# Kernel optimization log

Measured on AMD Instinct MI355X. Metric: run time of the kernel, lower is better.

The kernel has to match this reference:

```python
import jax, jax.numpy as jnp
import numpy as np

B_, L_ = 1, 1024
D_MODEL, D_INNER, D_XB = 2048, 4096, 1024
D_STATE = 16
DT_RANK = 128
INTER = 8192
EPS = 1e-5
GC = D_INNER // D_STATE   # 256 state groups (each covers D_STATE channels)
REP = D_INNER // D_XB     # 4: repeat_kv expansion factor for x and B


def setup_inputs() -> dict:
    key = jax.random.key(0)
    ks = jax.random.split(key, 8)
    s = 0.02
    return {
        "hidden_states": jax.random.normal(ks[0], (B_, L_, D_MODEL), jnp.float32),
        "rms1_w": jnp.ones((D_MODEL,), jnp.float32),
        "in_proj_w": jax.random.normal(ks[1], (2 * D_INNER + 2 * D_XB + DT_RANK, D_MODEL), jnp.float32) * s,
        "dt_proj_w": jax.random.normal(ks[2], (D_INNER, DT_RANK), jnp.float32) * s,
        "dt_proj_b": jax.random.normal(ks[3], (D_INNER,), jnp.float32) * 0.5 - 4.0,
        "A_log": jnp.tile(jnp.log(jnp.arange(1, D_STATE + 1, dtype=jnp.float32)), (D_INNER, 1)),
        "D_skip": jnp.ones((D_INNER,), jnp.float32),
        "out_proj_w": jax.random.normal(ks[4], (D_MODEL, D_INNER), jnp.float32) * s,
        "rms2_w": jnp.ones((D_MODEL,), jnp.float32),
        "gate_w": jax.random.normal(ks[5], (INTER, D_MODEL), jnp.float32) * s,
        "up_w": jax.random.normal(ks[6], (INTER, D_MODEL), jnp.float32) * s,
        "down_w": jax.random.normal(ks[7], (D_MODEL, INTER), jnp.float32) * s,
    }


def _rmsnorm(x, w):
    return x * jax.lax.rsqrt(jnp.mean(x * x, axis=-1, keepdims=True) + EPS) * w


def _mamba(x, in_proj_w, dt_proj_w, dt_proj_b, A_log, D_skip, out_proj_w):
    b, l, _ = x.shape
    zxbcdt = x @ in_proj_w.T  # (b,l, 2*d_inner + 2*d_xb + dt_rank)
    z = zxbcdt[..., :D_INNER]
    xv = zxbcdt[..., D_INNER:D_INNER + D_XB]
    Bm = zxbcdt[..., D_INNER + D_XB:D_INNER + 2 * D_XB]
    Cm = zxbcdt[..., D_INNER + 2 * D_XB:2 * D_INNER + 2 * D_XB]
    dt_in = zxbcdt[..., 2 * D_INNER + 2 * D_XB:]
    dt = jax.nn.softplus(dt_in @ dt_proj_w.T + dt_proj_b)  # (b,l,d_inner)
    # repeat_kv-style expansion of x and B from d_xb to d_inner (grouped by d_state)
    xg = jnp.repeat(xv.reshape(b, l, D_XB // D_STATE, D_STATE), REP, axis=2)  # (b,l,GC,n)
    Bg = jnp.repeat(Bm.reshape(b, l, D_XB // D_STATE, D_STATE), REP, axis=2)  # (b,l,GC,n)
    Cg = Cm.reshape(b, l, GC, D_STATE)                                        # (b,l,GC,n)
    x_full = xg.reshape(b, l, D_INNER)
    A = -jnp.exp(A_log)                       # (d_inner, n)
    dA = jnp.exp(dt[..., None] * A)           # (b,l,d_inner,n)
    dtx = (dt * x_full).reshape(b, l, GC, D_INNER // GC)  # channels per group == D_STATE here
    dBx = (dtx[..., :, None] * Bg[..., None, :]).reshape(b, l, D_INNER, D_STATE)

    def step(h, inp):
        dA_i, dBx_i, C_i = inp
        h = dA_i * h + dBx_i                  # (b,d_inner,n)
        # channel d in group d // D_STATE shares C of that group
        y = jnp.einsum('bgn,bgcn->bgc', C_i, h.reshape(b, GC, D_INNER // GC, D_STATE))
        return h, y.reshape(b, D_INNER)

    h0 = jnp.zeros((b, D_INNER, D_STATE), x.dtype)
    _, ys = jax.lax.scan(step, h0, (dA.transpose(1, 0, 2, 3), dBx.transpose(1, 0, 2, 3), Cg.transpose(1, 0, 2, 3)))
    y = ys.transpose(1, 0, 2) + D_skip * x_full
    y = y * jax.nn.silu(z)
    return y @ out_proj_w.T


def reference(hidden_states, rms1_w, in_proj_w, dt_proj_w, dt_proj_b, A_log, D_skip, out_proj_w, rms2_w, gate_w, up_w, down_w):
    res = hidden_states
    h = _rmsnorm(hidden_states, rms1_w)
    h = res + _mamba(h, in_proj_w, dt_proj_w, dt_proj_b, A_log, D_skip, out_proj_w)
    res = h
    hn = _rmsnorm(h, rms2_w)
    mlp = (jax.nn.silu(hn @ gate_w.T) * (hn @ up_w.T)) @ down_w.T
    return res + mlp
```

## Files before the change

kernel.cpp:

```cpp
#include <hip/hip_runtime.h>
#include <cstdint>
#include <cstddef>

#define L_SEQ   1024
#define DMODEL  2048
#define DINNER  4096
#define DXB     1024
#define DSTATE  16
#define DTRANK  128
#define INTER   8192
#define ZROW    10368
#define NCHUNK  16
#define CLEN    64

typedef __attribute__((ext_vector_type(8))) short  short8;
typedef __attribute__((ext_vector_type(4))) float  floatx4;
typedef unsigned short ushort_t;

__device__ __forceinline__ unsigned short f2bf(float f) {
  unsigned u = __float_as_uint(f);
  u += 0x7FFFu + ((u >> 16) & 1u);
  return (unsigned short)(u >> 16);
}
__device__ __forceinline__ float bf2f(unsigned short h) {
  return __uint_as_float(((unsigned)h) << 16);
}

__device__ __forceinline__ void gl_lds16(const void* g, void* l) {
  __builtin_amdgcn_global_load_lds(
      (const __attribute__((address_space(1))) unsigned int*)g,
      (__attribute__((address_space(3))) unsigned int*)l,
      16, 0, 0);
}

__global__ void __launch_bounds__(256) cvt_kernel(
    const float* __restrict__ src, ushort_t* __restrict__ dst, int n8)
{
  int idx = blockIdx.x * 256 + threadIdx.x;
  if (idx < n8) {
    const float4* s = (const float4*)src + (size_t)idx * 2;
    float4 v0 = s[0], v1 = s[1];
    union { ushort_t u[8]; uint4 v; } o;
    o.u[0] = f2bf(v0.x); o.u[1] = f2bf(v0.y); o.u[2] = f2bf(v0.z); o.u[3] = f2bf(v0.w);
    o.u[4] = f2bf(v1.x); o.u[5] = f2bf(v1.y); o.u[6] = f2bf(v1.z); o.u[7] = f2bf(v1.w);
    ((uint4*)dst)[idx] = o.v;
  }
}

template <int MI, int NI, int EPI, bool WF32>
__global__ void __launch_bounds__(256) gemm_bf16(
    const ushort_t* __restrict__ A, int lda,
    const ushort_t* __restrict__ W, int ldw,
    float* __restrict__ C, int ldc, int K,
    const float* __restrict__ aux,
    ushort_t* __restrict__ Cb, int col_lo, int ldcb)
{
  constexpr int BM = MI * 32, BN = NI * 32;
  constexpr int IA = BM / 64, IB = BN / 64;
  constexpr int ASZ = BM * 32, BSZ = BN * 32;
  __shared__ alignas(16) ushort_t As[2 * ASZ];
  __shared__ alignas(16) ushort_t Bs[2 * BSZ];

  const int kz = blockIdx.z;
  A += (size_t)kz * K;
  W += (size_t)kz * K;
  C += (size_t)kz * gridDim.y * BM * ldc;

  const int m0 = blockIdx.y * BM;
  const int n0 = blockIdx.x * BN;
  const int t = threadIdx.x;
  const int lane = t & 63, wave = t >> 6;
  const int wm = wave & 1, wn = wave >> 1;
  const int lrow = lane & 15, quad = lane >> 4;

  const int srow = wave * 16 + (lane >> 2);
  const int skof = (lane & 3) * 8;

  const ushort_t* gA[IA]; ushort_t* lA[IA];
  const ushort_t* gW[IB]; ushort_t* lB[IB];
#pragma unroll
  for (int j = 0; j < IA; ++j) {
    gA[j] = A + (size_t)(m0 + j * 64 + srow) * lda + skof;
    lA[j] = As + j * 2048 + wave * 512;
  }
#pragma unroll
  for (int j = 0; j < IB; ++j) {
    gW[j] = W + (size_t)(n0 + j * 64 + srow) * ldw + skof;
    lB[j] = Bs + j * 2048 + wave * 512;
  }

  floatx4 zero = {0.f, 0.f, 0.f, 0.f};
  floatx4 acc[MI][NI];
#pragma unroll
  for (int a = 0; a < MI; ++a)
#pragma unroll
    for (int b = 0; b < NI; ++b) acc[a][b] = zero;

#pragma unroll
  for (int j = 0; j < IA; ++j) gl_lds16(gA[j], lA[j]);
#pragma unroll
  for (int j = 0; j < IB; ++j) gl_lds16(gW[j], lB[j]);

  int buf = 0;
  for (int k0 = 0; k0 < K; k0 += 32) {
    __syncthreads();
    const int nk = k0 + 32;
    if (nk < K) {
      const int nb = buf ^ 1;
#pragma unroll
      for (int j = 0; j < IA; ++j) gl_lds16(gA[j] + nk, lA[j] + nb * ASZ);
#pragma unroll
      for (int j = 0; j < IB; ++j) gl_lds16(gW[j] + nk, lB[j] + nb * BSZ);
    }

    short8 af[MI], bf_[NI];
#pragma unroll
    for (int mi = 0; mi < MI; ++mi)
      af[mi] = *(const short8*)&As[buf * ASZ + (wm * (MI * 16) + mi * 16 + lrow) * 32 + quad * 8];
#pragma unroll
    for (int ni = 0; ni < NI; ++ni)
      bf_[ni] = *(const short8*)&Bs[buf * BSZ + (wn * (NI * 16) + ni * 16 + lrow) * 32 + quad * 8];
#pragma unroll
    for (int mi = 0; mi < MI; ++mi)
#pragma unroll
      for (int ni = 0; ni < NI; ++ni)
        acc[mi][ni] = __builtin_amdgcn_mfma_f32_16x16x32_bf16(af[mi], bf_[ni], acc[mi][ni], 0, 0, 0);
    buf ^= 1;
  }

#pragma unroll
  for (int mi = 0; mi < MI; ++mi)
#pragma unroll
    for (int ni = 0; ni < NI; ++ni)
#pragma unroll
      for (int reg = 0; reg < 4; ++reg) {
        int row = m0 + wm * (MI * 16) + mi * 16 + quad * 4 + reg;
        int col = n0 + wn * (NI * 16) + ni * 16 + lrow;
        float v = acc[mi][ni][reg];
        if (EPI == 1) {
          v += aux[col];
          v = (v > 20.f) ? v : log1pf(__expf(v));
        } else if (EPI == 2) {
          v += aux[(size_t)row * ldc + col];
        }
        if constexpr (WF32)
          C[(size_t)row * ldc + col] = v;
        if (Cb != nullptr && col >= col_lo)
          Cb[(size_t)row * ldcb + (col - col_lo)] = f2bf(v);
      }
}

template <int S>
__global__ void __launch_bounds__(256) reduce_add_kernel(
    const float* __restrict__ part, int stride4,
    const float* __restrict__ aux, float* __restrict__ out, int n4)
{
  int idx = blockIdx.x * 256 + threadIdx.x;
  if (idx < n4) {
    float4 v = ((const float4*)aux)[idx];
#pragma unroll
    for (int s = 0; s < S; ++s) {
      float4 p = ((const float4*)part)[(size_t)s * stride4 + idx];
      v.x += p.x; v.y += p.y; v.z += p.z; v.w += p.w;
    }
    ((float4*)out)[idx] = v;
  }
}

__global__ void __launch_bounds__(256) rmsnorm_kernel(
    const float* __restrict__ x, const float* __restrict__ w,
    ushort_t* __restrict__ out)
{
  const int row = blockIdx.x;
  const float* xr = x + (size_t)row * DMODEL;
  float ss = 0.f;
#pragma unroll
  for (int c = threadIdx.x * 4; c < DMODEL; c += 256 * 4) {
    float4 v = *(const float4*)(xr + c);
    ss += v.x * v.x + v.y * v.y + v.z * v.z + v.w * v.w;
  }
#pragma unroll
  for (int off = 32; off > 0; off >>= 1) ss += __shfl_down(ss, off);
  __shared__ float red[5];
  const int lane = threadIdx.x & 63, wv = threadIdx.x >> 6;
  if (lane == 0) red[wv] = ss;
  __syncthreads();
  if (threadIdx.x == 0)
    red[4] = rsqrtf((red[0] + red[1] + red[2] + red[3]) / (float)DMODEL + 1e-5f);
  __syncthreads();
  const float scale = red[4];
  ushort_t* orow = out + (size_t)row * DMODEL;
#pragma unroll
  for (int c = threadIdx.x * 4; c < DMODEL; c += 256 * 4) {
    float4 v  = *(const float4*)(xr + c);
    float4 w4 = *(const float4*)(w + c);
    ushort4 o;
    o.x = f2bf(v.x * scale * w4.x); o.y = f2bf(v.y * scale * w4.y);
    o.z = f2bf(v.z * scale * w4.z); o.w = f2bf(v.w * scale * w4.w);
    *(ushort4*)(orow + c) = o;
  }
}

__global__ void __launch_bounds__(256) scan_phase1(
    const float* __restrict__ zx, const float* __restrict__ dt,
    const float* __restrict__ A_log,
    float* __restrict__ hend, float* __restrict__ aprod)
{
  const int gt = blockIdx.x * 256 + threadIdx.x;
  const int cs = gt & 65535;
  const int c  = gt >> 16;
  const int i  = cs >> 4;
  const int n  = cs & 15;
  const int l0 = c * CLEN;
  const float a = -__expf(A_log[i * DSTATE + n]);

  const float* pdt = dt + (size_t)l0 * DINNER + i;
  const float* px  = zx + (size_t)l0 * ZROW + DINNER + ((i >> 6) << 4) + (i & 15);
  const float* pB  = zx + (size_t)l0 * ZROW + DINNER + DXB + ((i >> 6) << 4) + n;

  float h = 0.f, sdt = 0.f;
#pragma unroll 4
  for (int l = 0; l < CLEN; ++l) {
    const float d = pdt[(size_t)l * DINNER];
    const float x = px[(size_t)l * ZROW];
    const float B = pB[(size_t)l * ZROW];
    sdt += d;
    h = __expf(d * a) * h + (d * x) * B;
  }
  hend[gt]  = h;
  aprod[gt] = __expf(a * sdt);
}

__global__ void __launch_bounds__(256) scan_phase2(
    const float* __restrict__ hend, const float* __restrict__ aprod,
    float* __restrict__ hstart)
{
  const int cs = blockIdx.x * 256 + threadIdx.x;
  float H = 0.f;
#pragma unroll
  for (int c = 0; c < NCHUNK; ++c) {
    hstart[c * 65536 + cs] = H;
    H = aprod[c * 65536 + cs] * H + hend[c * 65536 + cs];
  }
}

__global__ void __launch_bounds__(256) scan_phase3(
    const float* __restrict__ zx, const float* __restrict__ dt,
    const float* __restrict__ A_log, const float* __restrict__ D_skip,
    const float* __restrict__ hstart,
    ushort_t* __restrict__ y)
{
  const int gt = blockIdx.x * 256 + threadIdx.x;
  const int cs = gt & 65535;
  const int c  = gt >> 16;
  const int i  = cs >> 4;
  const int n  = cs & 15;
  const int l0 = c * CLEN;
  const float a   = -__expf(A_log[i * DSTATE + n]);
  const float dsk = D_skip[i];

  const float* pdt = dt + (size_t)l0 * DINNER + i;
  const float* pz  = zx + (size_t)l0 * ZROW + i;
  const float* px  = zx + (size_t)l0 * ZROW + DINNER + ((i >> 6) << 4) + (i & 15);
  const float* pB  = zx + (size_t)l0 * ZROW + DINNER + DXB + ((i >> 6) << 4) + n;
  const float* pC  = zx + (size_t)l0 * ZROW + DINNER + 2 * DXB + (i & ~15) + n;
  ushort_t*    py  = y + (size_t)l0 * DINNER + i;

  float h = hstart[gt];
#pragma unroll 4
  for (int l = 0; l < CLEN; ++l) {
    const float d = pdt[(size_t)l * DINNER];
    const float x = px[(size_t)l * ZROW];
    const float z = pz[(size_t)l * ZROW];
    const float B = pB[(size_t)l * ZROW];
    const float C = pC[(size_t)l * ZROW];
    h = __expf(d * a) * h + (d * x) * B;
    float p = C * h;
    p += __shfl_xor(p, 1);
    p += __shfl_xor(p, 2);
    p += __shfl_xor(p, 4);
    p += __shfl_xor(p, 8);
    if (n == 0) {
      const float sz = z / (1.f + __expf(-z));
      py[(size_t)l * DINNER] = f2bf((p + dsk * x) * sz);
    }
  }
}

__global__ void __launch_bounds__(256) silu_mul_kernel(
    const ushort_t* __restrict__ g, const ushort_t* __restrict__ u,
    ushort_t* __restrict__ out, int n8)
{
  const int idx = blockIdx.x * 256 + threadIdx.x;
  if (idx < n8) {
    union { uint4 v; ushort_t u[8]; } gv, uv, ov;
    gv.v = ((const uint4*)g)[idx];
    uv.v = ((const uint4*)u)[idx];
#pragma unroll
    for (int j = 0; j < 8; ++j) {
      float gf = bf2f(gv.u[j]), uf = bf2f(uv.u[j]);
      ov.u[j] = f2bf(gf / (1.f + __expf(-gf)) * uf);
    }
    ((uint4*)out)[idx] = ov.v;
  }
}

extern "C" void kernel_launch(void* const* d_in, const int* in_sizes, int n_in,
                              void* d_out, int out_size, void* d_ws, size_t ws_size,
                              hipStream_t stream)
{
  const float* hidden    = (const float*)d_in[0];
  const float* rms1_w    = (const float*)d_in[1];
  const float* in_proj_w = (const float*)d_in[2];
  const float* dt_proj_w = (const float*)d_in[3];
  const float* dt_proj_b = (const float*)d_in[4];
  const float* A_log     = (const float*)d_in[5];
  const float* D_skip    = (const float*)d_in[6];
  const float* out_proj_w= (const float*)d_in[7];
  const float* rms2_w    = (const float*)d_in[8];
  const float* gate_w    = (const float*)d_in[9];
  const float* up_w      = (const float*)d_in[10];
  const float* down_w    = (const float*)d_in[11];
  float* out = (float*)d_out;

  char* ws = (char*)d_ws;
  ushort_t* h_norm_bf = (ushort_t*)(ws + 0);
  float*    h2        = (float*)   (ws + 4194304);
  ushort_t* hn_bf     = (ushort_t*)(ws + 12582912);
  float*    zxbcdt    = (float*)   (ws + 16777216);
  float*    part1     = (float*)   (ws + 16777216);
  ushort_t* up_bf     = (ushort_t*)(ws + 16777216);
  ushort_t* hm_bf     = (ushort_t*)(ws + 33554432);
  float*    dtbuf     = (float*)   (ws + 67108864);
  float*    hend_s    = (float*)   (ws + 83886080);
  float*    aprod_s   = (float*)   (ws + 88080384);
  float*    hstart_s  = (float*)   (ws + 92274688);
  ushort_t* gate_bf   = (ushort_t*)(ws + 67108864);
  float*    part2     = (float*)   (ws + 67108864);
  ushort_t* ybuf_bf   = (ushort_t*)(ws + 100663296);
  ushort_t* dtA_bf    = (ushort_t*)(ws + 109051904);
  ushort_t* wbuf      = (ushort_t*)(ws + 109314048);

  rmsnorm_kernel<<<L_SEQ, 256, 0, stream>>>(hidden, rms1_w, h_norm_bf);
  cvt_kernel<<<(ZROW * DMODEL / 8 + 255) / 256, 256, 0, stream>>>(in_proj_w, wbuf, ZROW * DMODEL / 8);
  gemm_bf16<4, 4, 0, true><<<dim3(ZROW / 128, L_SEQ / 128, 1), 256, 0, stream>>>(
      h_norm_bf, DMODEL, wbuf, DMODEL, zxbcdt, ZROW, DMODEL, nullptr,
      dtA_bf, 2 * DINNER + 2 * DXB, DTRANK);
  cvt_kernel<<<(DINNER * DTRANK / 8 + 255) / 256, 256, 0, stream>>>(dt_proj_w, wbuf, DINNER * DTRANK / 8);
  gemm_bf16<4, 4, 1, true><<<dim3(DINNER / 128, L_SEQ / 128, 1), 256, 0, stream>>>(
      dtA_bf, DTRANK, wbuf, DTRANK, dtbuf, DINNER, DTRANK, dt_proj_b,
      nullptr, 0, 0);
  scan_phase1<<<4096, 256, 0, stream>>>(zxbcdt, dtbuf, A_log, hend_s, aprod_s);
  scan_phase2<<<256, 256, 0, stream>>>(hend_s, aprod_s, hstart_s);
  scan_phase3<<<4096, 256, 0, stream>>>(zxbcdt, dtbuf, A_log, D_skip, hstart_s, ybuf_bf);
  cvt_kernel<<<(DMODEL * DINNER / 8 + 255) / 256, 256, 0, stream>>>(out_proj_w, wbuf, DMODEL * DINNER / 8);
  gemm_bf16<2, 4, 0, true><<<dim3(DMODEL / 128, L_SEQ / 64, 4), 256, 0, stream>>>(
      ybuf_bf, DINNER, wbuf, DINNER, part1, DMODEL, DINNER / 4, nullptr,
      nullptr, 0, 0);
  reduce_add_kernel<4><<<(L_SEQ * DMODEL / 4) / 256, 256, 0, stream>>>(
      part1, L_SEQ * DMODEL / 4, hidden, h2, L_SEQ * DMODEL / 4);
  rmsnorm_kernel<<<L_SEQ, 256, 0, stream>>>(h2, rms2_w, hn_bf);
  cvt_kernel<<<(INTER * DMODEL / 8 + 255) / 256, 256, 0, stream>>>(gate_w, wbuf, INTER * DMODEL / 8);
  gemm_bf16<4, 4, 0, false><<<dim3(INTER / 128, L_SEQ / 128, 1), 256, 0, stream>>>(
      hn_bf, DMODEL, wbuf, DMODEL, nullptr, INTER, DMODEL, nullptr,
      gate_bf, 0, INTER);
  cvt_kernel<<<(INTER * DMODEL / 8 + 255) / 256, 256, 0, stream>>>(up_w, wbuf, INTER * DMODEL / 8);
  gemm_bf16<4, 4, 0, false><<<dim3(INTER / 128, L_SEQ / 128, 1), 256, 0, stream>>>(
      hn_bf, DMODEL, wbuf, DMODEL, nullptr, INTER, DMODEL, nullptr,
      up_bf, 0, INTER);
  silu_mul_kernel<<<(L_SEQ * INTER / 8) / 256, 256, 0, stream>>>(
      gate_bf, up_bf, hm_bf, L_SEQ * INTER / 8);
  cvt_kernel<<<(DMODEL * INTER / 8 + 255) / 256, 256, 0, stream>>>(down_w, wbuf, DMODEL * INTER / 8);
  gemm_bf16<2, 4, 0, true><<<dim3(DMODEL / 128, L_SEQ / 64, 4), 256, 0, stream>>>(
      hm_bf, INTER, wbuf, INTER, part2, DMODEL, INTER / 4, nullptr,
      nullptr, 0, 0);
  reduce_add_kernel<4><<<(L_SEQ * DMODEL / 4) / 256, 256, 0, stream>>>(
      part2, L_SEQ * DMODEL / 4, h2, out, L_SEQ * DMODEL / 4);
}
```

Baseline: 760.5 us.

## Restructure selective scan per-channel with 16 states in registers, fuse reduce+rmsnorm

The scan kernels now assign one thread per channel holding all 16 state values in registers. B and C are loaded as float4 vectors and the output dot product is accumulated locally, which removes the cross-lane shuffles. Chunking changes from 16×64 to 64×16, and aprod is recomputed in phase2 from a per-chunk dt sum instead of being stored per state. The split-K reduction is fused with the second RMSNorm, the dt_proj GEMM switches to smaller tiles, and the workspace layout is reorganised. The costs are higher register pressure and a longer serial phase2 over 64 chunks.

```diff
diff --git a/kernel.cpp b/kernel.cpp
--- a/kernel.cpp
+++ b/kernel.cpp
@@ -10,8 +10,8 @@
 #define DTRANK  128
 #define INTER   8192
 #define ZROW    10368
-#define NCHUNK  16
-#define CLEN    64
+#define NCHUNK  64
+#define CLEN    16
 
 typedef __attribute__((ext_vector_type(8))) short  short8;
 typedef __attribute__((ext_vector_type(4))) float  floatx4;
@@ -140,8 +140,6 @@
         if (EPI == 1) {
           v += aux[col];
           v = (v > 20.f) ? v : log1pf(__expf(v));
-        } else if (EPI == 2) {
-          v += aux[(size_t)row * ldc + col];
         }
         if constexpr (WF32)
           C[(size_t)row * ldc + col] = v;
@@ -165,6 +163,48 @@
     }
     ((float4*)out)[idx] = v;
   }
+}
+
+__global__ void __launch_bounds__(256) reduce_rms_kernel(
+    const float* __restrict__ part, int stride,
+    const float* __restrict__ hidden,
+    const float* __restrict__ w,
+    float* __restrict__ h2, ushort_t* __restrict__ hn)
+{
+  const int row = blockIdx.x;
+  const int c0 = threadIdx.x * 8;
+  float4 v0 = *(const float4*)(hidden + (size_t)row * DMODEL + c0);
+  float4 v1 = *(const float4*)(hidden + (size_t)row * DMODEL + c0 + 4);
+#pragma unroll
+  for (int s = 0; s < 4; ++s) {
+    const float* p = part + (size_t)s * stride + (size_t)row * DMODEL + c0;
+    float4 p0 = *(const float4*)p;
+    float4 p1 = *(const float4*)(p + 4);
+    v0.x += p0.x; v0.y += p0.y; v0.z += p0.z; v0.w += p0.w;
+    v1.x += p1.x; v1.y += p1.y; v1.z += p1.z; v1.w += p1.w;
+  }
+  *(float4*)(h2 + (size_t)row * DMODEL + c0)     = v0;
+  *(float4*)(h2 + (size_t)row * DMODEL + c0 + 4) = v1;
+  float ss = v0.x*v0.x + v0.y*v0.y + v0.z*v0.z + v0.w*v0.w
+           + v1.x*v1.x + v1.y*v1.y + v1.z*v1.z + v1.w*v1.w;
+#pragma unroll
+  for (int off = 32; off > 0; off >>= 1) ss += __shfl_down(ss, off);
+  __shared__ float red[5];
+  const int lane = threadIdx.x & 63, wv = threadIdx.x >> 6;
+  if (lane == 0) red[wv] = ss;
+  __syncthreads();
+  if (threadIdx.x == 0)
+    red[4] = rsqrtf((red[0] + red[1] + red[2] + red[3]) / (float)DMODEL + 1e-5f);
+  __syncthreads();
+  const float scale = red[4];
+  float4 w0 = *(const float4*)(w + c0);
+  float4 w1 = *(const float4*)(w + c0 + 4);
+  union { ushort_t u[8]; uint4 q; } o;
+  o.u[0] = f2bf(v0.x * scale * w0.x); o.u[1] = f2bf(v0.y * scale * w0.y);
+  o.u[2] = f2bf(v0.z * scale * w0.z); o.u[3] = f2bf(v0.w * scale * w0.w);
+  o.u[4] = f2bf(v1.x * scale * w1.x); o.u[5] = f2bf(v1.y * scale * w1.y);
+  o.u[6] = f2bf(v1.z * scale * w1.z); o.u[7] = f2bf(v1.w * scale * w1.w);
+  *(uint4*)(hn + (size_t)row * DMODEL + c0) = o.q;
 }
 
 __global__ void __launch_bounds__(256) rmsnorm_kernel(
@@ -204,43 +244,69 @@
 __global__ void __launch_bounds__(256) scan_phase1(
     const float* __restrict__ zx, const float* __restrict__ dt,
     const float* __restrict__ A_log,
-    float* __restrict__ hend, float* __restrict__ aprod)
+    float* __restrict__ hend, float* __restrict__ sdtb)
 {
   const int gt = blockIdx.x * 256 + threadIdx.x;
-  const int cs = gt & 65535;
-  const int c  = gt >> 16;
-  const int i  = cs >> 4;
-  const int n  = cs & 15;
+  const int i  = gt & 4095;
+  const int c  = gt >> 12;
   const int l0 = c * CLEN;
-  const float a = -__expf(A_log[i * DSTATE + n]);
-
-  const float* pdt = dt + (size_t)l0 * DINNER + i;
-  const float* px  = zx + (size_t)l0 * ZROW + DINNER + ((i >> 6) << 4) + (i & 15);
-  const float* pB  = zx + (size_t)l0 * ZROW + DINNER + DXB + ((i >> 6) << 4) + n;
-
-  float h = 0.f, sdt = 0.f;
+
+  float a[16];
+  *(float4*)&a[0]  = *(const float4*)(A_log + i * 16 + 0);
+  *(float4*)&a[4]  = *(const float4*)(A_log + i * 16 + 4);
+  *(float4*)&a[8]  = *(const float4*)(A_log + i * 16 + 8);
+  *(float4*)&a[12] = *(const float4*)(A_log + i * 16 + 12);
+#pragma unroll
+  for (int n = 0; n < 16; ++n) a[n] = -__expf(a[n]);
+
+  float h[16];
+#pragma unroll
+  for (int n = 0; n < 16; ++n) h[n] = 0.f;
+  float sdt = 0.f;
+
+  const int xci = DINNER + ((i >> 6) << 4) + (i & 15);
+  const int bci = DINNER + DXB + ((i >> 6) << 4);
+  const float* zr = zx + (size_t)l0 * ZROW;
+  const float* dr = dt + (size_t)l0 * DINNER + i;
+
 #pragma unroll 4
   for (int l = 0; l < CLEN; ++l) {
-    const float d = pdt[(size_t)l * DINNER];
-    const float x = px[(size_t)l * ZROW];
-    const float B = pB[(size_t)l * ZROW];
+    const float* row = zr + l * ZROW;
+    const float d = dr[l * DINNER];
+    const float x = row[xci];
+    float B[16];
+    *(float4*)&B[0]  = *(const float4*)(row + bci);
+    *(float4*)&B[4]  = *(const float4*)(row + bci + 4);
+    *(float4*)&B[8]  = *(const float4*)(row + bci + 8);
+    *(float4*)&B[12] = *(const float4*)(row + bci + 12);
     sdt += d;
-    h = __expf(d * a) * h + (d * x) * B;
-  }
-  hend[gt]  = h;
-  aprod[gt] = __expf(a * sdt);
+    const float dtx = d * x;
+#pragma unroll
+    for (int n = 0; n < 16; ++n)
+      h[n] = __expf(d * a[n]) * h[n] + dtx * B[n];
+  }
+
+  float* he = hend + ((size_t)c * 65536 + i * 16);
+  *(float4*)(he + 0)  = *(float4*)&h[0];
+  *(float4*)(he + 4)  = *(float4*)&h[4];
+  *(float4*)(he + 8)  = *(float4*)&h[8];
+  *(float4*)(he + 12) = *(float4*)&h[12];
+  sdtb[c * 4096 + i] = sdt;
 }
 
 __global__ void __launch_bounds__(256) scan_phase2(
-    const float* __restrict__ hend, const float* __restrict__ aprod,
+    const float* __restrict__ hend, const float* __restrict__ sdtb,
+    const float* __restrict__ A_log,
     float* __restrict__ hstart)
 {
   const int cs = blockIdx.x * 256 + threadIdx.x;
+  const float a = -__expf(A_log[cs]);
+  const int i  = cs >> 4;
   float H = 0.f;
-#pragma unroll
+#pragma unroll 8
   for (int c = 0; c < NCHUNK; ++c) {
     hstart[c * 65536 + cs] = H;
-    H = aprod[c * 65536 + cs] * H + hend[c * 65536 + cs];
+    H = __expf(a * sdtb[c * 4096 + i]) * H + hend[c * 65536 + cs];
   }
 }
 
@@ -251,39 +317,64 @@
     ushort_t* __restrict__ y)
 {
   const int gt = blockIdx.x * 256 + threadIdx.x;
-  const int cs = gt & 65535;
-  const int c  = gt >> 16;
-  const int i  = cs >> 4;
-  const int n  = cs & 15;
+  const int i  = gt & 4095;
+  const int c  = gt >> 12;
   const int l0 = c * CLEN;
-  const float a   = -__expf(A_log[i * DSTATE + n]);
+
+  float a[16];
+  *(float4*)&a[0]  = *(const float4*)(A_log + i * 16 + 0);
+  *(float4*)&a[4]  = *(const float4*)(A_log + i * 16 + 4);
+  *(float4*)&a[8]  = *(const float4*)(A_log + i * 16 + 8);
+  *(float4*)&a[12] = *(const float4*)(A_log + i * 16 + 12);
+#pragma unroll
+  for (int n = 0; n < 16; ++n) a[n] = -__expf(a[n]);
   const float dsk = D_skip[i];
 
-  const float* pdt = dt + (size_t)l0 * DINNER + i;
-  const float* pz  = zx + (size_t)l0 * ZROW + i;
-  const float* px  = zx + (size_t)l0 * ZROW + DINNER + ((i >> 6) << 4) + (i & 15);
-  const float* pB  = zx + (size_t)l0 * ZROW + DINNER + DXB + ((i >> 6) << 4) + n;
-  const float* pC  = zx + (size_t)l0 * ZROW + DINNER + 2 * DXB + (i & ~15) + n;
-  ushort_t*    py  = y + (size_t)l0 * DINNER + i;
-
-  float h = hstart[gt];
-#pragma unroll 4
+  float h[16];
+  const float* hs = hstart + ((size_t)c * 65536 + i * 16);
+  *(float4*)&h[0]  = *(const float4*)(hs + 0);
+  *(float4*)&h[4]  = *(const float4*)(hs + 4);
+  *(float4*)&h[8]  = *(const float4*)(hs + 8);
+  *(float4*)&h[12] = *(const float4*)(hs + 12);
+
+  const int xci = DINNER + ((i >> 6) << 4) + (i & 15);
+  const int bci = DINNER + DXB + ((i >> 6) << 4);
+  const int cci = DINNER + 2 * DXB + (i & ~15);
+  const float* zr = zx + (size_t)l0 * ZROW;
+  const float* dr = dt + (size_t)l0 * DINNER + i;
+  ushort_t*    py = y + (size_t)l0 * DINNER + i;
+
+#pragma unroll 2
   for (int l = 0; l < CLEN; ++l) {
-    const float d = pdt[(size_t)l * DINNER];
-    const float x = px[(size_t)l * ZROW];
-    const float z = pz[(size_t)l * ZROW];
-    const float B = pB[(size_t)l * ZROW];
-    const float C = pC[(size_t)l * ZROW];
-    h = __expf(d * a) * h + (d * x) * B;
-    float p = C * h;
-    p += __shfl_xor(p, 1);
-    p += __shfl_xor(p, 2);
-    p += __shfl_xor(p, 4);
-    p += __shfl_xor(p, 8);
-    if (n == 0) {
-      const float sz = z / (1.f + __expf(-z));
-      py[(size_t)l * DINNER] = f2bf((p + dsk * x) * sz);
+    const float* row = zr + l * ZROW;
+    const float d = dr[l * DINNER];
+    const float x = row[xci];
+    const float z = row[i];
+    float B[16], C[16];
+    *(float4*)&B[0]  = *(const float4*)(row + bci);
+    *(float4*)&B[4]  = *(const float4*)(row + bci + 4);
+    *(float4*)&B[8]  = *(const float4*)(row + bci + 8);
+    *(float4*)&B[12] = *(const float4*)(row + bci + 12);
+    *(float4*)&C[0]  = *(const float4*)(row + cci);
+    *(float4*)&C[4]  = *(const float4*)(row + cci + 4);
+    *(float4*)&C[8]  = *(const float4*)(row + cci + 8);
+    *(float4*)&C[12] = *(const float4*)(row + cci + 12);
+    const float dtx = d * x;
+    float p0 = 0.f, p1 = 0.f, p2 = 0.f, p3 = 0.f;
+#pragma unroll
+    for (int n = 0; n < 4; ++n) {
+      h[n]      = __expf(d * a[n])      * h[n]      + dtx * B[n];
+      h[n + 4]  = __expf(d * a[n + 4])  * h[n + 4]  + dtx * B[n + 4];
+      h[n + 8]  = __expf(d * a[n + 8])  * h[n + 8]  + dtx * B[n + 8];
+      h[n + 12] = __expf(d * a[n + 12]) * h[n + 12] + dtx * B[n + 12];
+      p0 += C[n] * h[n];
+      p1 += C[n + 4] * h[n + 4];
+      p2 += C[n + 8] * h[n + 8];
+      p3 += C[n + 12] * h[n + 12];
     }
+    const float p = (p0 + p1) + (p2 + p3);
+    const float sz = z / (1.f + __expf(-z));
+    py[l * DINNER] = f2bf((p + dsk * x) * sz);
   }
 }
 
@@ -329,17 +420,17 @@
   ushort_t* hn_bf     = (ushort_t*)(ws + 12582912);
   float*    zxbcdt    = (float*)   (ws + 16777216);
   float*    part1     = (float*)   (ws + 16777216);
-  ushort_t* up_bf     = (ushort_t*)(ws + 16777216);
-  ushort_t* hm_bf     = (ushort_t*)(ws + 33554432);
+  ushort_t* gate_bf   = (ushort_t*)(ws + 16777216);
+  ushort_t* up_bf     = (ushort_t*)(ws + 33554432);
+  ushort_t* hm_bf     = (ushort_t*)(ws + 50331648);
   float*    dtbuf     = (float*)   (ws + 67108864);
+  float*    part2     = (float*)   (ws + 67108864);
   float*    hend_s    = (float*)   (ws + 83886080);
-  float*    aprod_s   = (float*)   (ws + 88080384);
-  float*    hstart_s  = (float*)   (ws + 92274688);
-  ushort_t* gate_bf   = (ushort_t*)(ws + 67108864);
-  float*    part2     = (float*)   (ws + 67108864);
-  ushort_t* ybuf_bf   = (ushort_t*)(ws + 100663296);
-  ushort_t* dtA_bf    = (ushort_t*)(ws + 109051904);
-  ushort_t* wbuf      = (ushort_t*)(ws + 109314048);
+  float*    hstart_s  = (float*)   (ws + 100663296);
+  float*    sdtb_s    = (float*)   (ws + 117440512);
+  ushort_t* ybuf_bf   = (ushort_t*)(ws + 118489088);
+  ushort_t* dtA_bf    = (ushort_t*)(ws + 126877696);
+  ushort_t* wbuf      = (ushort_t*)(ws + 127139840);
 
   rmsnorm_kernel<<<L_SEQ, 256, 0, stream>>>(hidden, rms1_w, h_norm_bf);
   cvt_kernel<<<(ZROW * DMODEL / 8 + 255) / 256, 256, 0, stream>>>(in_proj_w, wbuf, ZROW * DMODEL / 8);
@@ -347,19 +438,18 @@
       h_norm_bf, DMODEL, wbuf, DMODEL, zxbcdt, ZROW, DMODEL, nullptr,
       dtA_bf, 2 * DINNER + 2 * DXB, DTRANK);
   cvt_kernel<<<(DINNER * DTRANK / 8 + 255) / 256, 256, 0, stream>>>(dt_proj_w, wbuf, DINNER * DTRANK / 8);
-  gemm_bf16<4, 4, 1, true><<<dim3(DINNER / 128, L_SEQ / 128, 1), 256, 0, stream>>>(
+  gemm_bf16<2, 4, 1, true><<<dim3(DINNER / 128, L_SEQ / 64, 1), 256, 0, stream>>>(
       dtA_bf, DTRANK, wbuf, DTRANK, dtbuf, DINNER, DTRANK, dt_proj_b,
       nullptr, 0, 0);
-  scan_phase1<<<4096, 256, 0, stream>>>(zxbcdt, dtbuf, A_log, hend_s, aprod_s);
-  scan_phase2<<<256, 256, 0, stream>>>(hend_s, aprod_s, hstart_s);
-  scan_phase3<<<4096, 256, 0, stream>>>(zxbcdt, dtbuf, A_log, D_skip, hstart_s, ybuf_bf);
+  scan_phase1<<<1024, 256, 0, stream>>>(zxbcdt, dtbuf, A_log, hend_s, sdtb_s);
+  scan_phase2<<<256, 256, 0, stream>>>(hend_s, sdtb_s, A_log, hstart_s);
+  scan_phase3<<<1024, 256, 0, stream>>>(zxbcdt, dtbuf, A_log, D_skip, hstart_s, ybuf_bf);
   cvt_kernel<<<(DMODEL * DINNER / 8 + 255) / 256, 256, 0, stream>>>(out_proj_w, wbuf, DMODEL * DINNER / 8);
   gemm_bf16<2, 4, 0, true><<<dim3(DMODEL / 128, L_SEQ / 64, 4), 256, 0, stream>>>(
       ybuf_bf, DINNER, wbuf, DINNER, part1, DMODEL, DINNER / 4, nullptr,
       nullptr, 0, 0);
-  reduce_add_kernel<4><<<(L_SEQ * DMODEL / 4) / 256, 256, 0, stream>>>(
-      part1, L_SEQ * DMODEL / 4, hidden, h2, L_SEQ * DMODEL / 4);
-  rmsnorm_kernel<<<L_SEQ, 256, 0, stream>>>(h2, rms2_w, hn_bf);
+  reduce_rms_kernel<<<L_SEQ, 256, 0, stream>>>(
+      part1, L_SEQ * DMODEL, hidden, rms2_w, h2, hn_bf);
   cvt_kernel<<<(INTER * DMODEL / 8 + 255) / 256, 256, 0, stream>>>(gate_w, wbuf, INTER * DMODEL / 8);
   gemm_bf16<4, 4, 0, false><<<dim3(INTER / 128, L_SEQ / 128, 1), 256, 0, stream>>>(
       hn_bf, DMODEL, wbuf, DMODEL, nullptr, INTER, DMODEL, nullptr,
```

Result: faster. 680.5 us (-10.5%).
